# Performance work log

Hardware: AMD Instinct MI355X
Metric: run time of the kernel (lower is better)

Reference implementation:

```python
import jax, jax.numpy as jnp
import numpy as np

TOP_K = 8
N_EXPERTS = 256
N_GROUP = 8
TOPK_GROUP = 4
ROUTED_SCALING = 2.5
NORM_TOPK_PROB = True
HIDDEN = 4096
TOKENS = 16384


def setup_inputs() -> dict:
    key = jax.random.key(0)
    k1, k2, k3 = jax.random.split(key, 3)
    hidden_states = jax.random.normal(k1, (TOKENS, HIDDEN), dtype=jnp.float32)
    weight = jax.random.normal(k2, (N_EXPERTS, HIDDEN), dtype=jnp.float32) * 0.02
    e_score_correction_bias = jax.random.normal(k3, (N_EXPERTS,), dtype=jnp.float32) * 0.1
    return {
        "hidden_states": hidden_states,
        "weight": weight,
        "e_score_correction_bias": e_score_correction_bias,
    }


def _get_topk_indices(scores, bias):
    # scores: [T, E]
    T = scores.shape[0]
    scores_for_choice = scores + bias[None, :]                      # [T, E]
    grp = scores_for_choice.reshape(T, N_GROUP, N_EXPERTS // N_GROUP)
    top2_vals, _ = jax.lax.top_k(grp, 2)                            # [T, G, 2]
    group_scores = top2_vals.sum(axis=-1)                           # [T, G]
    _, group_idx = jax.lax.top_k(group_scores, TOPK_GROUP)          # [T, topk_group]
    group_mask = jnp.zeros((T, N_GROUP), dtype=scores.dtype)
    group_mask = jnp.take_along_axis(group_mask, group_idx, axis=1)  # placeholder, replaced below
    # scatter 1s into selected groups
    group_mask = jnp.zeros((T, N_GROUP), dtype=bool)
    group_mask = group_mask.at[jnp.arange(T)[:, None], group_idx].set(True)
    score_mask = jnp.repeat(group_mask, N_EXPERTS // N_GROUP, axis=1)  # [T, E]
    masked = jnp.where(score_mask, scores_for_choice, 0.0)
    _, topk_indices = jax.lax.top_k(masked, TOP_K)                  # [T, top_k]
    return topk_indices


def reference(hidden_states, weight, e_score_correction_bias):
    # router logits: [T, E]
    router_logits = jnp.einsum("th,eh->te", hidden_states.astype(jnp.float32),
                               weight.astype(jnp.float32))
    scores = jax.nn.sigmoid(router_logits)
    topk_indices = _get_topk_indices(scores, e_score_correction_bias)
    topk_weights = jnp.take_along_axis(scores, topk_indices, axis=1)  # [T, top_k]
    if NORM_TOPK_PROB:
        denom = topk_weights.sum(axis=-1, keepdims=True) + 1e-20
        topk_weights = topk_weights / denom
    topk_weights = topk_weights * ROUTED_SCALING
    return topk_indices, topk_weights.astype(jnp.float32)
```

## Files before the change

kernel.cpp:

```cpp
#include <hip/hip_runtime.h>
#include <math.h>

#define T_TOKENS 16384
#define HID      4096
#define NEXP     256
#define NGROUP   8
#define GSIZE    32
#define TOPKG    4
#define TOPK     8
#define RSCALE   2.5f

#define TAU   2e-5f
#define TAUG  3e-5f

#define BM     64
#define BK     32
#define SPLITK 4
#define KSPAN  (HID / SPLITK)
#define NKS    (KSPAN / BK)
#define NSG    (HID / BK)

#define A_HI   0
#define A_LO   2048
#define B_HI   4096
#define B_LO   12288
#define STG_TOT 20480

#define WQ_LIMB (NSG * 8192)

typedef __attribute__((ext_vector_type(8))) short bf16x8;
typedef __attribute__((ext_vector_type(4))) float f32x4;

__device__ __forceinline__ int stoffA(int r, int q) {
    return (r >> 4) * 512 + (q >> 1) * 128 + (r & 15) * 8 + (q & 1) * 4;
}
__device__ __forceinline__ int froffL(int lane) {
    return (lane >> 4) * 128 + (lane & 15) * 8;
}

__device__ __forceinline__ void gload16(const void* g, void* l) {
    __builtin_amdgcn_global_load_lds(
        (const __attribute__((address_space(1))) void*)g,
        (__attribute__((address_space(3))) void*)l, 16, 0, 0);
}

__device__ __forceinline__ void split4(const float4 v, uint& h01, uint& h23,
                                       uint& l01, uint& l23) {
    const uint u0 = __float_as_uint(v.x) + 0x8000u;
    const uint u1 = __float_as_uint(v.y) + 0x8000u;
    const uint u2 = __float_as_uint(v.z) + 0x8000u;
    const uint u3 = __float_as_uint(v.w) + 0x8000u;
    h01 = __builtin_amdgcn_perm(u1, u0, 0x07060302u);
    h23 = __builtin_amdgcn_perm(u3, u2, 0x07060302u);
    const float f0 = v.x - __uint_as_float(u0 & 0xFFFF0000u);
    const float f1 = v.y - __uint_as_float(u1 & 0xFFFF0000u);
    const float f2 = v.z - __uint_as_float(u2 & 0xFFFF0000u);
    const float f3 = v.w - __uint_as_float(u3 & 0xFFFF0000u);
    l01 = __builtin_amdgcn_perm(__float_as_uint(f1) + 0x8000u,
                                __float_as_uint(f0) + 0x8000u, 0x07060302u);
    l23 = __builtin_amdgcn_perm(__float_as_uint(f3) + 0x8000u,
                                __float_as_uint(f2) + 0x8000u, 0x07060302u);
}

template <class SC>
__device__ __forceinline__ bool route_core(SC sc, const float* __restrict__ bias,
                                           int* id, float* wv)
{
    float gs[NGROUP];
#pragma unroll
    for (int g = 0; g < NGROUP; ++g) {
        float m1 = -1e30f, m2 = -1e30f;
        for (int i = 0; i < GSIZE; ++i) {
            const int e = g * GSIZE + i;
            const float v = sc(e) + bias[e];
            if (v > m1)      { m2 = m1; m1 = v; }
            else if (v > m2) { m2 = v; }
        }
        gs[g] = m1 + m2;
    }

    unsigned gmask = 0;
    float g4 = -1e30f;
#pragma unroll
    for (int r = 0; r < TOPKG; ++r) {
        int bi = 0; float bv = -1e30f;
#pragma unroll
        for (int g = 0; g < NGROUP; ++g) {
            const bool taken = (gmask >> g) & 1;
            if (!taken && gs[g] > bv) { bv = gs[g]; bi = g; }
        }
        gmask |= 1u << bi;
        g4 = bv;
    }
    float g5 = -1e30f;
#pragma unroll
    for (int g = 0; g < NGROUP; ++g)
        if (!((gmask >> g) & 1) && gs[g] > g5) g5 = gs[g];

    float val[TOPK + 1]; int vid[TOPK + 1];
#pragma unroll
    for (int r = 0; r <= TOPK; ++r) { val[r] = -1e30f; vid[r] = 0; }
    for (int e = 0; e < NEXP; ++e) {
        const bool allowed = (gmask >> (e >> 5)) & 1;
        const float v = allowed ? (sc(e) + bias[e]) : 0.0f;
        if (v > val[TOPK]) {
#pragma unroll
            for (int p = TOPK; p >= 1; --p) {
                if (v > val[p - 1])  { val[p] = val[p - 1]; vid[p] = vid[p - 1]; }
                else if (v > val[p]) { val[p] = v;          vid[p] = e; }
            }
            if (v > val[0]) { val[0] = v; vid[0] = e; }
        }
    }

    bool tight = (g4 - g5 < TAUG);
#pragma unroll
    for (int i = 0; i < TOPK; ++i) tight |= (val[i] - val[i + 1] < TAU);

    float sum = 0.0f;
#pragma unroll
    for (int r = 0; r < TOPK; ++r) { id[r] = vid[r]; wv[r] = sc(vid[r]); sum += wv[r]; }
    const float inv = RSCALE / (sum + 1e-20f);
#pragma unroll
    for (int r = 0; r < TOPK; ++r) wv[r] *= inv;
    return tight;
}

__device__ void exact_token(const float* __restrict__ hs, const float* __restrict__ wt,
                            const float* __restrict__ bias, float* __restrict__ out, int t)
{
    float lg[NEXP];
    const float* hrow = hs + (size_t)t * HID;
    for (int e = 0; e < NEXP; ++e) {
        const float* wr = wt + (size_t)e * HID;
        float a = 0.0f;
        for (int k = 0; k < HID; k += 4) {
            const float4 x = *(const float4*)(hrow + k);
            const float4 b = *(const float4*)(wr + k);
            a = fmaf(x.x, b.x, a); a = fmaf(x.y, b.y, a);
            a = fmaf(x.z, b.z, a); a = fmaf(x.w, b.w, a);
        }
        lg[e] = 1.0f / (1.0f + expf(-a));
    }
    int id[TOPK]; float wv[TOPK];
    route_core([&](int e) { return lg[e]; }, bias, id, wv);
    for (int r = 0; r < TOPK; ++r) {
        out[(size_t)t * TOPK + r] = (float)id[r];
        out[(size_t)T_TOKENS * TOPK + (size_t)t * TOPK + r] = wv[r];
    }
}

__global__ __launch_bounds__(256, 8)
void conv_weight(const float* __restrict__ wt, ushort* __restrict__ wq)
{
    const int g  = blockIdx.x * 256 + threadIdx.x;
    const int e  = g >> 9;
    const int kc = g & 511;
    const int sg  = kc >> 2;
    const int kch = kc & 3;

    const float4 v0 = *(const float4*)(wt + (size_t)e * HID + kc * 8);
    const float4 v1 = *(const float4*)(wt + (size_t)e * HID + kc * 8 + 4);
    uint h01, h23, l01, l23, h45, h67, l45, l67;
    split4(v0, h01, h23, l01, l23);
    split4(v1, h45, h67, l45, l67);

    const size_t idx = (size_t)sg * 8192 + (size_t)((e >> 4) * 512 + kch * 128 + (e & 15) * 8);
    uint4 hv; hv.x = h01; hv.y = h23; hv.z = h45; hv.w = h67;
    uint4 lv; lv.x = l01; lv.y = l23; lv.z = l45; lv.w = l67;
    *(uint4*)&wq[idx] = hv;
    *(uint4*)&wq[(size_t)WQ_LIMB + idx] = lv;
}

__global__ __launch_bounds__(256, 4)
void router_gemm(const float* __restrict__ hs, const ushort* __restrict__ wq,
                 float* __restrict__ pw)
{
    __shared__ ushort u16[STG_TOT];

    const int tid  = threadIdx.x;
    const int lane = tid & 63;
    const int w    = tid >> 6;
    const int m    = blockIdx.x >> 2;
    const int sk   = blockIdx.x & 3;
    const int t0   = m * BM;
    const int kb0  = sk * KSPAN;
    const int r0   = tid >> 3;
    const int q    = tid & 7;

    const ushort* wq_hi = wq;
    const ushort* wq_lo = wq + WQ_LIMB;

    f32x4 acc[4][4];
#pragma unroll
    for (int i = 0; i < 4; ++i)
#pragma unroll
        for (int j = 0; j < 4; ++j) acc[i][j] = (f32x4)0.0f;

    float4 ra[2];
#pragma unroll
    for (int s = 0; s < 2; ++s)
        ra[s] = *(const float4*)(hs + (size_t)(t0 + r0 + 32 * s) * HID + kb0 + q * 4);

    for (int ks = 0; ks < NKS; ++ks) {
        const int sg = sk * NKS + ks;
        __syncthreads();

        {
            const size_t gb = (size_t)sg * 8192 + (size_t)(w * 4) * 512 + (size_t)lane * 8;
#pragma unroll
            for (int i = 0; i < 4; ++i) {
                gload16(wq_hi + gb + i * 512, &u16[B_HI + (w * 4 + i) * 512]);
                gload16(wq_lo + gb + i * 512, &u16[B_LO + (w * 4 + i) * 512]);
            }
        }
#pragma unroll
        for (int s = 0; s < 2; ++s) {
            const int r = r0 + 32 * s;
            uint h01, h23, l01, l23;
            split4(ra[s], h01, h23, l01, l23);
            const int eo = stoffA(r, q);
            uint2 hv; hv.x = h01; hv.y = h23;
            uint2 lv; lv.x = l01; lv.y = l23;
            *(uint2*)&u16[A_HI + eo] = hv;
            *(uint2*)&u16[A_LO + eo] = lv;
        }
        __syncthreads();

        if (ks + 1 < NKS) {
            const int kb = kb0 + (ks + 1) * BK;
#pragma unroll
            for (int s = 0; s < 2; ++s)
                ra[s] = *(const float4*)(hs + (size_t)(t0 + r0 + 32 * s) * HID + kb + q * 4);
        }

        const int fo = froffL(lane);
        bf16x8 ah[4], al[4];
#pragma unroll
        for (int rt = 0; rt < 4; ++rt) {
            ah[rt] = *(const bf16x8*)&u16[A_HI + rt * 512 + fo];
            al[rt] = *(const bf16x8*)&u16[A_LO + rt * 512 + fo];
        }
#pragma unroll
        for (int c = 0; c < 4; ++c) {
            const int ct = w * 4 + c;
            const bf16x8 bh = *(const bf16x8*)&u16[B_HI + ct * 512 + fo];
            const bf16x8 bl = *(const bf16x8*)&u16[B_LO + ct * 512 + fo];
#pragma unroll
            for (int rt = 0; rt < 4; ++rt) {
                acc[rt][c] = __builtin_amdgcn_mfma_f32_16x16x32_bf16(ah[rt], bh, acc[rt][c], 0, 0, 0);
                acc[rt][c] = __builtin_amdgcn_mfma_f32_16x16x32_bf16(ah[rt], bl, acc[rt][c], 0, 0, 0);
                acc[rt][c] = __builtin_amdgcn_mfma_f32_16x16x32_bf16(al[rt], bh, acc[rt][c], 0, 0, 0);
            }
        }
    }

#pragma unroll
    for (int rt = 0; rt < 4; ++rt)
#pragma unroll
        for (int c = 0; c < 4; ++c) {
            const int col  = w * 64 + c * 16 + (lane & 15);
            const int rowb = rt * 16 + (lane >> 4) * 4;
#pragma unroll
            for (int j = 0; j < 4; ++j)
                pw[((size_t)(sk * T_TOKENS) + t0 + rowb + j) * NEXP + col] = acc[rt][c][j];
        }
}

__global__ __launch_bounds__(256, 2)
void router_route(const float* __restrict__ pw, const float* __restrict__ bias,
                  float* __restrict__ out,
                  unsigned* __restrict__ wcnt, unsigned* __restrict__ wlist,
                  unsigned cap)
{
    __shared__ float Lg[NEXP * 64];
    const int tid = threadIdx.x;
    const int t0  = blockIdx.x * 64;

#pragma unroll 8
    for (int t = 0; t < 64; ++t) {
        float v = 0.0f;
#pragma unroll
        for (int s = 0; s < SPLITK; ++s)
            v += pw[((size_t)(s * T_TOKENS) + t0 + t) * NEXP + tid];
        Lg[tid * 64 + ((t + tid) & 63)] = 1.0f / (1.0f + expf(-v));
    }
    __syncthreads();

    if (tid < 64) {
        const int t = t0 + tid;
        int id[TOPK]; float wv[TOPK];
        const bool tight = route_core(
            [&](int e) { return Lg[e * 64 + ((tid + e) & 63)]; }, bias, id, wv);

#pragma unroll
        for (int r = 0; r < TOPK; ++r) {
            out[(size_t)t * TOPK + r] = (float)id[r];
            out[(size_t)T_TOKENS * TOPK + (size_t)t * TOPK + r] = wv[r];
        }
        if (tight) {
            const unsigned pos = atomicAdd(wcnt, 1u);
            if (pos < cap) wlist[pos] = (unsigned)t;
        }
    }
}

__global__ __launch_bounds__(256, 4)
void router_exact(const float* __restrict__ hs, const float* __restrict__ wt,
                  const float* __restrict__ bias, float* __restrict__ out,
                  const unsigned* __restrict__ wcnt, const unsigned* __restrict__ wlist,
                  unsigned cap)
{
    __shared__ float hrow[HID];
    __shared__ float lg[NEXP];
    const unsigned count = min(*wcnt, cap);
    const int tid  = threadIdx.x;
    const int lane = tid & 63;
    const int w    = tid >> 6;

    for (unsigned b = blockIdx.x; b < count; b += gridDim.x) {
        __syncthreads();
        const int t = (int)wlist[b];

#pragma unroll
        for (int i = 0; i < 4; ++i) {
            const int f4 = i * 256 + tid;
            *(float4*)&hrow[f4 * 4] = *(const float4*)(hs + (size_t)t * HID + f4 * 4);
        }
        __syncthreads();

        for (int g = 0; g < 16; ++g) {
            const int e0 = w * 64 + g * 4;
            float a[4] = {0.0f, 0.0f, 0.0f, 0.0f};
#pragma unroll 4
            for (int j = 0; j < 16; ++j) {
                const int f4 = j * 64 + lane;
                const float4 h = *(const float4*)&hrow[f4 * 4];
#pragma unroll
                for (int p = 0; p < 4; ++p) {
                    const float4 v = *(const float4*)(wt + (size_t)(e0 + p) * HID + f4 * 4);
                    a[p] = fmaf(h.x, v.x, a[p]); a[p] = fmaf(h.y, v.y, a[p]);
                    a[p] = fmaf(h.z, v.z, a[p]); a[p] = fmaf(h.w, v.w, a[p]);
                }
            }
#pragma unroll
            for (int p = 0; p < 4; ++p)
#pragma unroll
                for (int d = 1; d < 64; d <<= 1)
                    a[p] += __shfl_xor(a[p], d, 64);
            if (lane == 0) {
#pragma unroll
                for (int p = 0; p < 4; ++p)
                    lg[e0 + p] = 1.0f / (1.0f + expf(-a[p]));
            }
        }
        __syncthreads();

        if (tid == 0) {
            int id[TOPK]; float wv[TOPK];
            route_core([&](int e) { return lg[e]; }, bias, id, wv);
            for (int r = 0; r < TOPK; ++r) {
                out[(size_t)t * TOPK + r] = (float)id[r];
                out[(size_t)T_TOKENS * TOPK + (size_t)t * TOPK + r] = wv[r];
            }
        }
    }
}

__global__ __launch_bounds__(512, 1)
void router_mono(const float* __restrict__ hs, const float* __restrict__ wt,
                 const float* __restrict__ bias, float* __restrict__ out,
                 unsigned* __restrict__ wcnt, unsigned* __restrict__ wlist, unsigned cap)
{
    __shared__ float smem[16384];
    ushort* u16 = (ushort*)smem;
    float*  Lg  = smem;

    const int tid  = threadIdx.x;
    const int lane = tid & 63;
    const int w    = tid >> 6;
    const int t0   = blockIdx.x * 64;
    const int ar   = tid >> 3;
    const int aq   = tid & 7;

    f32x4 acc[4][2];
#pragma unroll
    for (int i = 0; i < 4; ++i)
#pragma unroll
        for (int j = 0; j < 2; ++j) acc[i][j] = (f32x4)0.0f;

    float4 ra, rb[4];
    ra = *(const float4*)(hs + (size_t)(t0 + ar) * HID + aq * 4);
#pragma unroll
    for (int s = 0; s < 4; ++s)
        rb[s] = *(const float4*)(wt + (size_t)(ar + s * 64) * HID + aq * 4);

    for (int ks = 0; ks < HID / BK; ++ks) {
        __syncthreads();
        {
            uint h01, h23, l01, l23;
            split4(ra, h01, h23, l01, l23);
            const int eo = stoffA(ar, aq);
            uint2 hv; hv.x = h01; hv.y = h23;
            uint2 lv; lv.x = l01; lv.y = l23;
            *(uint2*)&u16[0 + eo] = hv;
            *(uint2*)&u16[2048 + eo] = lv;
        }
#pragma unroll
        for (int s = 0; s < 4; ++s) {
            const int e = ar + s * 64;
            uint h01, h23, l01, l23;
            split4(rb[s], h01, h23, l01, l23);
            const int eo = stoffA(e, aq);
            uint2 hv; hv.x = h01; hv.y = h23;
            uint2 lv; lv.x = l01; lv.y = l23;
            *(uint2*)&u16[4096 + eo] = hv;
            *(uint2*)&u16[12288 + eo] = lv;
        }
        __syncthreads();
        if (ks + 1 < HID / BK) {
            const int k0 = (ks + 1) * BK;
            ra = *(const float4*)(hs + (size_t)(t0 + ar) * HID + k0 + aq * 4);
#pragma unroll
            for (int s = 0; s < 4; ++s)
                rb[s] = *(const float4*)(wt + (size_t)(ar + s * 64) * HID + k0 + aq * 4);
        }
        const int fo = froffL(lane);
        bf16x8 ah[4], al[4];
#pragma unroll
        for (int rt = 0; rt < 4; ++rt) {
            ah[rt] = *(const bf16x8*)&u16[0 + rt * 512 + fo];
            al[rt] = *(const bf16x8*)&u16[2048 + rt * 512 + fo];
        }
#pragma unroll
        for (int c = 0; c < 2; ++c) {
            const int ct = w * 2 + c;
            const bf16x8 bh = *(const bf16x8*)&u16[4096 + ct * 512 + fo];
            const bf16x8 bl = *(const bf16x8*)&u16[12288 + ct * 512 + fo];
#pragma unroll
            for (int rt = 0; rt < 4; ++rt) {
                acc[rt][c] = __builtin_amdgcn_mfma_f32_16x16x32_bf16(ah[rt], bh, acc[rt][c], 0, 0, 0);
                acc[rt][c] = __builtin_amdgcn_mfma_f32_16x16x32_bf16(ah[rt], bl, acc[rt][c], 0, 0, 0);
                acc[rt][c] = __builtin_amdgcn_mfma_f32_16x16x32_bf16(al[rt], bh, acc[rt][c], 0, 0, 0);
            }
        }
    }
    __syncthreads();
#pragma unroll
    for (int rt = 0; rt < 4; ++rt)
#pragma unroll
        for (int c = 0; c < 2; ++c) {
            const int col  = w * 32 + c * 16 + (lane & 15);
            const int rowb = rt * 16 + (lane >> 4) * 4;
#pragma unroll
            for (int j = 0; j < 4; ++j) {
                const int row = rowb + j;
                Lg[col * 64 + ((row + col) & 63)] = 1.0f / (1.0f + expf(-acc[rt][c][j]));
            }
        }
    __syncthreads();

    if (tid < 64) {
        const int t = t0 + tid;
        int id[TOPK]; float wv[TOPK];
        const bool tight = route_core(
            [&](int e) { return Lg[e * 64 + ((tid + e) & 63)]; }, bias, id, wv);
#pragma unroll
        for (int r = 0; r < TOPK; ++r) {
            out[(size_t)t * TOPK + r] = (float)id[r];
            out[(size_t)T_TOKENS * TOPK + (size_t)t * TOPK + r] = wv[r];
        }
        if (tight) {
            bool queued = false;
            if (wcnt) {
                const unsigned pos = atomicAdd(wcnt, 1u);
                if (pos < cap) { wlist[pos] = (unsigned)t; queued = true; }
            }
            if (!queued) exact_token(hs, wt, bias, out, t);
        }
    }
}

extern "C" void kernel_launch(void* const* d_in, const int* in_sizes, int n_in,
                              void* d_out, int out_size, void* d_ws, size_t ws_size,
                              hipStream_t stream) {
    const float* hs   = (const float*)d_in[0];
    const float* wt   = (const float*)d_in[1];
    const float* bias = (const float*)d_in[2];
    float* out = (float*)d_out;
    (void)in_sizes; (void)n_in; (void)out_size;

    const size_t PW_BYTES = (size_t)SPLITK * T_TOKENS * NEXP * 4;
    const size_t WQ_BYTES = (size_t)2 * WQ_LIMB * 2;
    const size_t NEED = PW_BYTES + WQ_BYTES + 4 + (size_t)T_TOKENS * 4;

    if (ws_size >= NEED) {
        float*    pw    = (float*)d_ws;
        ushort*   wq    = (ushort*)((char*)d_ws + PW_BYTES);
        unsigned* wcnt  = (unsigned*)((char*)d_ws + PW_BYTES + WQ_BYTES);
        unsigned* wlist = wcnt + 1;
        hipMemsetAsync(wcnt, 0, sizeof(unsigned), stream);
        conv_weight<<<512, 256, 0, stream>>>(wt, wq);
        router_gemm<<<(T_TOKENS / BM) * SPLITK, 256, 0, stream>>>(hs, wq, pw);
        router_route<<<T_TOKENS / 64, 256, 0, stream>>>(pw, bias, out, wcnt, wlist,
                                                        (unsigned)T_TOKENS);
        router_exact<<<2048, 256, 0, stream>>>(hs, wt, bias, out, wcnt, wlist,
                                               (unsigned)T_TOKENS);
    } else if (ws_size >= 8) {
        unsigned cap = (unsigned)((ws_size - 4) / 4);
        if (cap > T_TOKENS) cap = T_TOKENS;
        unsigned* wcnt  = (unsigned*)d_ws;
        unsigned* wlist = wcnt + 1;
        hipMemsetAsync(d_ws, 0, sizeof(unsigned), stream);
        router_mono<<<T_TOKENS / 64, 512, 0, stream>>>(hs, wt, bias, out, wcnt, wlist, cap);
        router_exact<<<2048, 256, 0, stream>>>(hs, wt, bias, out, wcnt, wlist, cap);
    } else {
        router_mono<<<T_TOKENS / 64, 512, 0, stream>>>(hs, wt, bias, out,
                                                       nullptr, nullptr, 0u);
    }
}
```

Before: 357.2 us.

## Fuse routing into split-K GEMM with last-block reduction and double-buffered LDS

Fuses the routing kernel into the GEMM: the last split-K block for each tile, found through an atomic counter, sums the partials, applies the sigmoid and runs top-k. This removes a separate kernel launch and some partial-sum traffic. Split-K drops from 4 to 2 and LDS staging becomes double-buffered, so the next tile's loads overlap with the MFMA work, which is also wrapped in s_setprio. The cost is twice the LDS, lower occupancy (launch bounds go from 4 to 2), fewer blocks, and a serialized tail in which the last block of each tile does the routing.

```diff
diff --git a/kernel.cpp b/kernel.cpp
--- a/kernel.cpp
+++ b/kernel.cpp
@@ -15,16 +15,17 @@
 
 #define BM     64
 #define BK     32
-#define SPLITK 4
+#define SPLITK 2
 #define KSPAN  (HID / SPLITK)
 #define NKS    (KSPAN / BK)
 #define NSG    (HID / BK)
+#define NMT    (T_TOKENS / BM)
 
 #define A_HI   0
 #define A_LO   2048
 #define B_HI   4096
 #define B_LO   12288
-#define STG_TOT 20480
+#define BUFSZ  20480
 
 #define WQ_LIMB (NSG * 8192)
 
@@ -172,17 +173,20 @@
     *(uint4*)&wq[(size_t)WQ_LIMB + idx] = lv;
 }
 
-__global__ __launch_bounds__(256, 4)
+__global__ __launch_bounds__(256, 2)
 void router_gemm(const float* __restrict__ hs, const ushort* __restrict__ wq,
-                 float* __restrict__ pw)
+                 const float* __restrict__ bias,
+                 float* __restrict__ pw, float* __restrict__ out,
+                 unsigned* __restrict__ cntm,
+                 unsigned* __restrict__ wcnt, unsigned* __restrict__ wlist, unsigned cap)
 {
-    __shared__ ushort u16[STG_TOT];
+    __shared__ ushort u16[2 * BUFSZ];
 
     const int tid  = threadIdx.x;
     const int lane = tid & 63;
     const int w    = tid >> 6;
-    const int m    = blockIdx.x >> 2;
-    const int sk   = blockIdx.x & 3;
+    const int m    = blockIdx.x >> 1;
+    const int sk   = blockIdx.x & 1;
     const int t0   = m * BM;
     const int kb0  = sk * KSPAN;
     const int r0   = tid >> 3;
@@ -198,54 +202,75 @@
         for (int j = 0; j < 4; ++j) acc[i][j] = (f32x4)0.0f;
 
     float4 ra[2];
-#pragma unroll
-    for (int s = 0; s < 2; ++s)
-        ra[s] = *(const float4*)(hs + (size_t)(t0 + r0 + 32 * s) * HID + kb0 + q * 4);
-
-    for (int ks = 0; ks < NKS; ++ks) {
-        const int sg = sk * NKS + ks;
-        __syncthreads();
-
-        {
-            const size_t gb = (size_t)sg * 8192 + (size_t)(w * 4) * 512 + (size_t)lane * 8;
-#pragma unroll
-            for (int i = 0; i < 4; ++i) {
-                gload16(wq_hi + gb + i * 512, &u16[B_HI + (w * 4 + i) * 512]);
-                gload16(wq_lo + gb + i * 512, &u16[B_LO + (w * 4 + i) * 512]);
-            }
+    {
+        const int sg0 = sk * NKS;
+        const size_t gb = (size_t)sg0 * 8192 + (size_t)(w * 4) * 512 + (size_t)lane * 8;
+#pragma unroll
+        for (int i = 0; i < 4; ++i) {
+            gload16(wq_hi + gb + i * 512, &u16[B_HI + (w * 4 + i) * 512]);
+            gload16(wq_lo + gb + i * 512, &u16[B_LO + (w * 4 + i) * 512]);
         }
 #pragma unroll
         for (int s = 0; s < 2; ++s) {
-            const int r = r0 + 32 * s;
+            const float4 v = *(const float4*)(hs + (size_t)(t0 + r0 + 32 * s) * HID + kb0 + q * 4);
             uint h01, h23, l01, l23;
-            split4(ra[s], h01, h23, l01, l23);
-            const int eo = stoffA(r, q);
+            split4(v, h01, h23, l01, l23);
+            const int eo = stoffA(r0 + 32 * s, q);
             uint2 hv; hv.x = h01; hv.y = h23;
             uint2 lv; lv.x = l01; lv.y = l23;
             *(uint2*)&u16[A_HI + eo] = hv;
             *(uint2*)&u16[A_LO + eo] = lv;
         }
-        __syncthreads();
+#pragma unroll
+        for (int s = 0; s < 2; ++s)
+            ra[s] = *(const float4*)(hs + (size_t)(t0 + r0 + 32 * s) * HID + kb0 + BK + q * 4);
+    }
+    __syncthreads();
+
+    int cur = 0;
+    for (int ks = 0; ks < NKS; ++ks) {
+        ushort* bc = u16 + cur * BUFSZ;
+        ushort* bn = u16 + (cur ^ 1) * BUFSZ;
 
         if (ks + 1 < NKS) {
-            const int kb = kb0 + (ks + 1) * BK;
-#pragma unroll
-            for (int s = 0; s < 2; ++s)
-                ra[s] = *(const float4*)(hs + (size_t)(t0 + r0 + 32 * s) * HID + kb + q * 4);
+            const int sg = sk * NKS + ks + 1;
+            const size_t gb = (size_t)sg * 8192 + (size_t)(w * 4) * 512 + (size_t)lane * 8;
+#pragma unroll
+            for (int i = 0; i < 4; ++i) {
+                gload16(wq_hi + gb + i * 512, bn + B_HI + (w * 4 + i) * 512);
+                gload16(wq_lo + gb + i * 512, bn + B_LO + (w * 4 + i) * 512);
+            }
+#pragma unroll
+            for (int s = 0; s < 2; ++s) {
+                uint h01, h23, l01, l23;
+                split4(ra[s], h01, h23, l01, l23);
+                const int eo = stoffA(r0 + 32 * s, q);
+                uint2 hv; hv.x = h01; hv.y = h23;
+                uint2 lv; lv.x = l01; lv.y = l23;
+                *(uint2*)&bn[A_HI + eo] = hv;
+                *(uint2*)&bn[A_LO + eo] = lv;
+            }
+            if (ks + 2 < NKS) {
+                const int kb = kb0 + (ks + 2) * BK;
+#pragma unroll
+                for (int s = 0; s < 2; ++s)
+                    ra[s] = *(const float4*)(hs + (size_t)(t0 + r0 + 32 * s) * HID + kb + q * 4);
+            }
         }
 
         const int fo = froffL(lane);
         bf16x8 ah[4], al[4];
 #pragma unroll
         for (int rt = 0; rt < 4; ++rt) {
-            ah[rt] = *(const bf16x8*)&u16[A_HI + rt * 512 + fo];
-            al[rt] = *(const bf16x8*)&u16[A_LO + rt * 512 + fo];
-        }
+            ah[rt] = *(const bf16x8*)&bc[A_HI + rt * 512 + fo];
+            al[rt] = *(const bf16x8*)&bc[A_LO + rt * 512 + fo];
+        }
+        __builtin_amdgcn_s_setprio(1);
 #pragma unroll
         for (int c = 0; c < 4; ++c) {
             const int ct = w * 4 + c;
-            const bf16x8 bh = *(const bf16x8*)&u16[B_HI + ct * 512 + fo];
-            const bf16x8 bl = *(const bf16x8*)&u16[B_LO + ct * 512 + fo];
+            const bf16x8 bh = *(const bf16x8*)&bc[B_HI + ct * 512 + fo];
+            const bf16x8 bl = *(const bf16x8*)&bc[B_LO + ct * 512 + fo];
 #pragma unroll
             for (int rt = 0; rt < 4; ++rt) {
                 acc[rt][c] = __builtin_amdgcn_mfma_f32_16x16x32_bf16(ah[rt], bh, acc[rt][c], 0, 0, 0);
@@ -253,6 +278,10 @@
                 acc[rt][c] = __builtin_amdgcn_mfma_f32_16x16x32_bf16(al[rt], bh, acc[rt][c], 0, 0, 0);
             }
         }
+        __builtin_amdgcn_s_setprio(0);
+
+        __syncthreads();
+        cur ^= 1;
     }
 
 #pragma unroll
@@ -265,42 +294,40 @@
             for (int j = 0; j < 4; ++j)
                 pw[((size_t)(sk * T_TOKENS) + t0 + rowb + j) * NEXP + col] = acc[rt][c][j];
         }
-}
-
-__global__ __launch_bounds__(256, 2)
-void router_route(const float* __restrict__ pw, const float* __restrict__ bias,
-                  float* __restrict__ out,
-                  unsigned* __restrict__ wcnt, unsigned* __restrict__ wlist,
-                  unsigned cap)
-{
-    __shared__ float Lg[NEXP * 64];
-    const int tid = threadIdx.x;
-    const int t0  = blockIdx.x * 64;
-
+
+    __threadfence();
+    __syncthreads();
+    volatile int* flag = (volatile int*)(u16 + 2 * BUFSZ - 2);
+    if (tid == 0) {
+        const unsigned old = atomicAdd(&cntm[m], 1u);
+        *flag = (old == SPLITK - 1) ? 1 : 0;
+    }
+    __syncthreads();
+    if (*flag) {
+        __threadfence();
+        float* Lg = (float*)u16;
 #pragma unroll 8
-    for (int t = 0; t < 64; ++t) {
-        float v = 0.0f;
-#pragma unroll
-        for (int s = 0; s < SPLITK; ++s)
-            v += pw[((size_t)(s * T_TOKENS) + t0 + t) * NEXP + tid];
-        Lg[tid * 64 + ((t + tid) & 63)] = 1.0f / (1.0f + expf(-v));
-    }
-    __syncthreads();
-
-    if (tid < 64) {
-        const int t = t0 + tid;
-        int id[TOPK]; float wv[TOPK];
-        const bool tight = route_core(
-            [&](int e) { return Lg[e * 64 + ((tid + e) & 63)]; }, bias, id, wv);
-
-#pragma unroll
-        for (int r = 0; r < TOPK; ++r) {
-            out[(size_t)t * TOPK + r] = (float)id[r];
-            out[(size_t)T_TOKENS * TOPK + (size_t)t * TOPK + r] = wv[r];
-        }
-        if (tight) {
-            const unsigned pos = atomicAdd(wcnt, 1u);
-            if (pos < cap) wlist[pos] = (unsigned)t;
+        for (int t = 0; t < BM; ++t) {
+            const float v = pw[((size_t)(0 * T_TOKENS) + t0 + t) * NEXP + tid]
+                          + pw[((size_t)(1 * T_TOKENS) + t0 + t) * NEXP + tid];
+            Lg[tid * 64 + ((t + tid) & 63)] = 1.0f / (1.0f + expf(-v));
+        }
+        __syncthreads();
+
+        if (tid < BM) {
+            const int t = t0 + tid;
+            int id[TOPK]; float wv[TOPK];
+            const bool tight = route_core(
+                [&](int e) { return Lg[e * 64 + ((tid + e) & 63)]; }, bias, id, wv);
+#pragma unroll
+            for (int r = 0; r < TOPK; ++r) {
+                out[(size_t)t * TOPK + r] = (float)id[r];
+                out[(size_t)T_TOKENS * TOPK + (size_t)t * TOPK + r] = wv[r];
+            }
+            if (tight) {
+                const unsigned pos = atomicAdd(wcnt, 1u);
+                if (pos < cap) wlist[pos] = (unsigned)t;
+            }
         }
     }
 }
@@ -490,20 +517,22 @@
     float* out = (float*)d_out;
     (void)in_sizes; (void)n_in; (void)out_size;
 
-    const size_t PW_BYTES = (size_t)SPLITK * T_TOKENS * NEXP * 4;
-    const size_t WQ_BYTES = (size_t)2 * WQ_LIMB * 2;
-    const size_t NEED = PW_BYTES + WQ_BYTES + 4 + (size_t)T_TOKENS * 4;
+    const size_t PW_BYTES  = (size_t)SPLITK * T_TOKENS * NEXP * 4;
+    const size_t WQ_BYTES  = (size_t)2 * WQ_LIMB * 2;
+    const size_t CTL_BYTES = 4 + (size_t)NMT * 4;
+    const size_t NEED = PW_BYTES + WQ_BYTES + CTL_BYTES + (size_t)T_TOKENS * 4;
 
     if (ws_size >= NEED) {
         float*    pw    = (float*)d_ws;
         ushort*   wq    = (ushort*)((char*)d_ws + PW_BYTES);
         unsigned* wcnt  = (unsigned*)((char*)d_ws + PW_BYTES + WQ_BYTES);
-        unsigned* wlist = wcnt + 1;
-        hipMemsetAsync(wcnt, 0, sizeof(unsigned), stream);
+        unsigned* cntm  = wcnt + 1;
+        unsigned* wlist = cntm + NMT;
+        hipMemsetAsync(wcnt, 0, CTL_BYTES, stream);
         conv_weight<<<512, 256, 0, stream>>>(wt, wq);
-        router_gemm<<<(T_TOKENS / BM) * SPLITK, 256, 0, stream>>>(hs, wq, pw);
-        router_route<<<T_TOKENS / 64, 256, 0, stream>>>(pw, bias, out, wcnt, wlist,
-                                                        (unsigned)T_TOKENS);
+        router_gemm<<<NMT * SPLITK, 256, 0, stream>>>(hs, wq, bias, pw, out,
+                                                      cntm, wcnt, wlist,
+                                                      (unsigned)T_TOKENS);
         router_exact<<<2048, 256, 0, stream>>>(hs, wt, bias, out, wcnt, wlist,
                                                (unsigned)T_TOKENS);
     } else if (ws_size >= 8) {
```

Result: slower. 472.6 us (+32.3%).

## Load GEMM operands directly into registers and batch exact-recheck tokens

Applied to the files above, without the earlier changes.

The router GEMM drops LDS staging and its two barriers per K step. Each wave now loads its pre-split bf16 weight fragments from global memory and builds the hidden-state hi/lo fragments in registers, so each wave re-reads hidden rows that other waves also read. The exact fallback kernel processes four flagged tokens per block so each weight load is reused across four rows, at the cost of more shared memory and lower occupancy. Launch bounds are lowered to match the higher register use.

```diff
diff --git a/kernel.cpp b/kernel.cpp
--- a/kernel.cpp
+++ b/kernel.cpp
@@ -20,29 +20,10 @@
 #define NKS    (KSPAN / BK)
 #define NSG    (HID / BK)
 
-#define A_HI   0
-#define A_LO   2048
-#define B_HI   4096
-#define B_LO   12288
-#define STG_TOT 20480
-
 #define WQ_LIMB (NSG * 8192)
 
 typedef __attribute__((ext_vector_type(8))) short bf16x8;
 typedef __attribute__((ext_vector_type(4))) float f32x4;
-
-__device__ __forceinline__ int stoffA(int r, int q) {
-    return (r >> 4) * 512 + (q >> 1) * 128 + (r & 15) * 8 + (q & 1) * 4;
-}
-__device__ __forceinline__ int froffL(int lane) {
-    return (lane >> 4) * 128 + (lane & 15) * 8;
-}
-
-__device__ __forceinline__ void gload16(const void* g, void* l) {
-    __builtin_amdgcn_global_load_lds(
-        (const __attribute__((address_space(1))) void*)g,
-        (__attribute__((address_space(3))) void*)l, 16, 0, 0);
-}
 
 __device__ __forceinline__ void split4(const float4 v, uint& h01, uint& h23,
                                        uint& l01, uint& l23) {
@@ -172,12 +153,10 @@
     *(uint4*)&wq[(size_t)WQ_LIMB + idx] = lv;
 }
 
-__global__ __launch_bounds__(256, 4)
+__global__ __launch_bounds__(256, 3)
 void router_gemm(const float* __restrict__ hs, const ushort* __restrict__ wq,
                  float* __restrict__ pw)
 {
-    __shared__ ushort u16[STG_TOT];
-
     const int tid  = threadIdx.x;
     const int lane = tid & 63;
     const int w    = tid >> 6;
@@ -185,8 +164,9 @@
     const int sk   = blockIdx.x & 3;
     const int t0   = m * BM;
     const int kb0  = sk * KSPAN;
-    const int r0   = tid >> 3;
-    const int q    = tid & 7;
+
+    const int row = lane & 15;
+    const int kq  = lane >> 4;
 
     const ushort* wq_hi = wq;
     const ushort* wq_lo = wq + WQ_LIMB;
@@ -197,62 +177,41 @@
 #pragma unroll
         for (int j = 0; j < 4; ++j) acc[i][j] = (f32x4)0.0f;
 
-    float4 ra[2];
-#pragma unroll
-    for (int s = 0; s < 2; ++s)
-        ra[s] = *(const float4*)(hs + (size_t)(t0 + r0 + 32 * s) * HID + kb0 + q * 4);
-
     for (int ks = 0; ks < NKS; ++ks) {
         const int sg = sk * NKS + ks;
-        __syncthreads();
-
-        {
-            const size_t gb = (size_t)sg * 8192 + (size_t)(w * 4) * 512 + (size_t)lane * 8;
-#pragma unroll
-            for (int i = 0; i < 4; ++i) {
-                gload16(wq_hi + gb + i * 512, &u16[B_HI + (w * 4 + i) * 512]);
-                gload16(wq_lo + gb + i * 512, &u16[B_LO + (w * 4 + i) * 512]);
-            }
-        }
-#pragma unroll
-        for (int s = 0; s < 2; ++s) {
-            const int r = r0 + 32 * s;
-            uint h01, h23, l01, l23;
-            split4(ra[s], h01, h23, l01, l23);
-            const int eo = stoffA(r, q);
-            uint2 hv; hv.x = h01; hv.y = h23;
-            uint2 lv; lv.x = l01; lv.y = l23;
-            *(uint2*)&u16[A_HI + eo] = hv;
-            *(uint2*)&u16[A_LO + eo] = lv;
-        }
-        __syncthreads();
-
-        if (ks + 1 < NKS) {
-            const int kb = kb0 + (ks + 1) * BK;
-#pragma unroll
-            for (int s = 0; s < 2; ++s)
-                ra[s] = *(const float4*)(hs + (size_t)(t0 + r0 + 32 * s) * HID + kb + q * 4);
-        }
-
-        const int fo = froffL(lane);
+        const int kb = kb0 + ks * BK;
+
+        bf16x8 bh[4], bl[4];
+        const size_t bb = (size_t)sg * 8192 + (size_t)(w * 4) * 512 + (size_t)lane * 8;
+#pragma unroll
+        for (int c = 0; c < 4; ++c) {
+            bh[c] = *(const bf16x8*)(wq_hi + bb + c * 512);
+            bl[c] = *(const bf16x8*)(wq_lo + bb + c * 512);
+        }
+
         bf16x8 ah[4], al[4];
 #pragma unroll
         for (int rt = 0; rt < 4; ++rt) {
-            ah[rt] = *(const bf16x8*)&u16[A_HI + rt * 512 + fo];
-            al[rt] = *(const bf16x8*)&u16[A_LO + rt * 512 + fo];
-        }
-#pragma unroll
-        for (int c = 0; c < 4; ++c) {
-            const int ct = w * 4 + c;
-            const bf16x8 bh = *(const bf16x8*)&u16[B_HI + ct * 512 + fo];
-            const bf16x8 bl = *(const bf16x8*)&u16[B_LO + ct * 512 + fo];
+            const float* ap = hs + (size_t)(t0 + rt * 16 + row) * HID + kb + kq * 8;
+            const float4 v0 = *(const float4*)ap;
+            const float4 v1 = *(const float4*)(ap + 4);
+            uint h01, h23, l01, l23, h45, h67, l45, l67;
+            split4(v0, h01, h23, l01, l23);
+            split4(v1, h45, h67, l45, l67);
+            uint4 hv; hv.x = h01; hv.y = h23; hv.z = h45; hv.w = h67;
+            uint4 lv; lv.x = l01; lv.y = l23; lv.z = l45; lv.w = l67;
+            ah[rt] = *(const bf16x8*)&hv;
+            al[rt] = *(const bf16x8*)&lv;
+        }
+
+#pragma unroll
+        for (int c = 0; c < 4; ++c)
 #pragma unroll
             for (int rt = 0; rt < 4; ++rt) {
-                acc[rt][c] = __builtin_amdgcn_mfma_f32_16x16x32_bf16(ah[rt], bh, acc[rt][c], 0, 0, 0);
-                acc[rt][c] = __builtin_amdgcn_mfma_f32_16x16x32_bf16(ah[rt], bl, acc[rt][c], 0, 0, 0);
-                acc[rt][c] = __builtin_amdgcn_mfma_f32_16x16x32_bf16(al[rt], bh, acc[rt][c], 0, 0, 0);
-            }
-        }
+                acc[rt][c] = __builtin_amdgcn_mfma_f32_16x16x32_bf16(ah[rt], bh[c], acc[rt][c], 0, 0, 0);
+                acc[rt][c] = __builtin_amdgcn_mfma_f32_16x16x32_bf16(ah[rt], bl[c], acc[rt][c], 0, 0, 0);
+                acc[rt][c] = __builtin_amdgcn_mfma_f32_16x16x32_bf16(al[rt], bh[c], acc[rt][c], 0, 0, 0);
+            }
     }
 
 #pragma unroll
@@ -305,60 +264,86 @@
     }
 }
 
-__global__ __launch_bounds__(256, 4)
+__global__ __launch_bounds__(256, 2)
 void router_exact(const float* __restrict__ hs, const float* __restrict__ wt,
                   const float* __restrict__ bias, float* __restrict__ out,
                   const unsigned* __restrict__ wcnt, const unsigned* __restrict__ wlist,
                   unsigned cap)
 {
-    __shared__ float hrow[HID];
-    __shared__ float lg[NEXP];
+    __shared__ float hrow[4][HID];
+    __shared__ float lg[4][NEXP + 1];
     const unsigned count = min(*wcnt, cap);
     const int tid  = threadIdx.x;
     const int lane = tid & 63;
     const int w    = tid >> 6;
 
-    for (unsigned b = blockIdx.x; b < count; b += gridDim.x) {
+    for (unsigned base = blockIdx.x * 4u; base < count; base += gridDim.x * 4u) {
         __syncthreads();
-        const int t = (int)wlist[b];
-
-#pragma unroll
-        for (int i = 0; i < 4; ++i) {
-            const int f4 = i * 256 + tid;
-            *(float4*)&hrow[f4 * 4] = *(const float4*)(hs + (size_t)t * HID + f4 * 4);
+        const unsigned n = (count - base < 4u) ? (count - base) : 4u;
+        int toks[4];
+#pragma unroll
+        for (int s = 0; s < 4; ++s)
+            toks[s] = (int)wlist[base + (((unsigned)s < n - 1) ? (unsigned)s : (n - 1))];
+
+#pragma unroll
+        for (int s = 0; s < 4; ++s) {
+            const float* hr = hs + (size_t)toks[s] * HID;
+#pragma unroll
+            for (int i = 0; i < 4; ++i) {
+                const int f4 = i * 256 + tid;
+                *(float4*)&hrow[s][f4 * 4] = *(const float4*)(hr + f4 * 4);
+            }
         }
         __syncthreads();
 
         for (int g = 0; g < 16; ++g) {
             const int e0 = w * 64 + g * 4;
-            float a[4] = {0.0f, 0.0f, 0.0f, 0.0f};
+            float a[4][4];
+#pragma unroll
+            for (int p = 0; p < 4; ++p)
+#pragma unroll
+                for (int t = 0; t < 4; ++t) a[p][t] = 0.0f;
+
 #pragma unroll 4
             for (int j = 0; j < 16; ++j) {
                 const int f4 = j * 64 + lane;
-                const float4 h = *(const float4*)&hrow[f4 * 4];
+                float4 h[4];
+#pragma unroll
+                for (int t = 0; t < 4; ++t)
+                    h[t] = *(const float4*)&hrow[t][f4 * 4];
 #pragma unroll
                 for (int p = 0; p < 4; ++p) {
                     const float4 v = *(const float4*)(wt + (size_t)(e0 + p) * HID + f4 * 4);
-                    a[p] = fmaf(h.x, v.x, a[p]); a[p] = fmaf(h.y, v.y, a[p]);
-                    a[p] = fmaf(h.z, v.z, a[p]); a[p] = fmaf(h.w, v.w, a[p]);
+#pragma unroll
+                    for (int t = 0; t < 4; ++t) {
+                        a[p][t] = fmaf(h[t].x, v.x, a[p][t]);
+                        a[p][t] = fmaf(h[t].y, v.y, a[p][t]);
+                        a[p][t] = fmaf(h[t].z, v.z, a[p][t]);
+                        a[p][t] = fmaf(h[t].w, v.w, a[p][t]);
+                    }
                 }
             }
 #pragma unroll
             for (int p = 0; p < 4; ++p)
 #pragma unroll
-                for (int d = 1; d < 64; d <<= 1)
-                    a[p] += __shfl_xor(a[p], d, 64);
+                for (int t = 0; t < 4; ++t)
+#pragma unroll
+                    for (int d = 1; d < 64; d <<= 1)
+                        a[p][t] += __shfl_xor(a[p][t], d, 64);
             if (lane == 0) {
 #pragma unroll
-                for (int p = 0; p < 4; ++p)
-                    lg[e0 + p] = 1.0f / (1.0f + expf(-a[p]));
+                for (int t = 0; t < 4; ++t)
+#pragma unroll
+                    for (int p = 0; p < 4; ++p)
+                        lg[t][e0 + p] = 1.0f / (1.0f + expf(-a[p][t]));
             }
         }
         __syncthreads();
 
-        if (tid == 0) {
+        if (tid < (int)n) {
+            const int t = toks[tid];
             int id[TOPK]; float wv[TOPK];
-            route_core([&](int e) { return lg[e]; }, bias, id, wv);
+            route_core([&](int e) { return lg[tid][e]; }, bias, id, wv);
             for (int r = 0; r < TOPK; ++r) {
                 out[(size_t)t * TOPK + r] = (float)id[r];
                 out[(size_t)T_TOKENS * TOPK + (size_t)t * TOPK + r] = wv[r];
@@ -400,7 +385,7 @@
         {
             uint h01, h23, l01, l23;
             split4(ra, h01, h23, l01, l23);
-            const int eo = stoffA(ar, aq);
+            const int eo = (ar >> 4) * 512 + (aq >> 1) * 128 + (ar & 15) * 8 + (aq & 1) * 4;
             uint2 hv; hv.x = h01; hv.y = h23;
             uint2 lv; lv.x = l01; lv.y = l23;
             *(uint2*)&u16[0 + eo] = hv;
@@ -411,7 +396,7 @@
             const int e = ar + s * 64;
             uint h01, h23, l01, l23;
             split4(rb[s], h01, h23, l01, l23);
-            const int eo = stoffA(e, aq);
+            const int eo = (e >> 4) * 512 + (aq >> 1) * 128 + (e & 15) * 8 + (aq & 1) * 4;
             uint2 hv; hv.x = h01; hv.y = h23;
             uint2 lv; lv.x = l01; lv.y = l23;
             *(uint2*)&u16[4096 + eo] = hv;
@@ -425,7 +410,7 @@
             for (int s = 0; s < 4; ++s)
                 rb[s] = *(const float4*)(wt + (size_t)(ar + s * 64) * HID + k0 + aq * 4);
         }
-        const int fo = froffL(lane);
+        const int fo = (lane >> 4) * 128 + (lane & 15) * 8;
         bf16x8 ah[4], al[4];
 #pragma unroll
         for (int rt = 0; rt < 4; ++rt) {
```

Result: slower. 536.2 us (+50.1%).

## Fuse split-K reduction and routing into GEMM via last-arriver atomic counter

Applied to the files above, without the earlier changes.

Removes the separate router_route launch. The last split-K block for each token tile, found through a per-tile atomic counter, now sums the partials, applies sigmoid and runs grouped top-k inside the GEMM kernel, reusing its shared staging buffer in two 32-token halves. This cuts one kernel launch and lets routing overlap with other tiles' GEMM work, at the cost of threadfences, extra atomics and a serialized tail in the last-arriving block. The ambiguity thresholds TAU and TAUG are also tightened, so fewer tokens should fall back to the exact recompute path, with some risk to correctness margin.

```diff
diff --git a/kernel.cpp b/kernel.cpp
--- a/kernel.cpp
+++ b/kernel.cpp
@@ -10,8 +10,8 @@
 #define TOPK     8
 #define RSCALE   2.5f
 
-#define TAU   2e-5f
-#define TAUG  3e-5f
+#define TAU   1.5e-5f
+#define TAUG  2.5e-5f
 
 #define BM     64
 #define BK     32
@@ -19,12 +19,14 @@
 #define KSPAN  (HID / SPLITK)
 #define NKS    (KSPAN / BK)
 #define NSG    (HID / BK)
+#define NMT    (T_TOKENS / BM)
 
 #define A_HI   0
 #define A_LO   2048
 #define B_HI   4096
 #define B_LO   12288
 #define STG_TOT 20480
+#define FLAG_U16 20476
 
 #define WQ_LIMB (NSG * 8192)
 
@@ -174,7 +176,10 @@
 
 __global__ __launch_bounds__(256, 4)
 void router_gemm(const float* __restrict__ hs, const ushort* __restrict__ wq,
-                 float* __restrict__ pw)
+                 const float* __restrict__ bias,
+                 float* __restrict__ pw, float* __restrict__ out,
+                 unsigned* __restrict__ cntm,
+                 unsigned* __restrict__ wcnt, unsigned* __restrict__ wlist, unsigned cap)
 {
     __shared__ ushort u16[STG_TOT];
 
@@ -265,42 +270,47 @@
             for (int j = 0; j < 4; ++j)
                 pw[((size_t)(sk * T_TOKENS) + t0 + rowb + j) * NEXP + col] = acc[rt][c][j];
         }
-}
-
-__global__ __launch_bounds__(256, 2)
-void router_route(const float* __restrict__ pw, const float* __restrict__ bias,
-                  float* __restrict__ out,
-                  unsigned* __restrict__ wcnt, unsigned* __restrict__ wlist,
-                  unsigned cap)
-{
-    __shared__ float Lg[NEXP * 64];
-    const int tid = threadIdx.x;
-    const int t0  = blockIdx.x * 64;
-
+
+    __threadfence();
+    __syncthreads();
+    volatile int* flag = (volatile int*)&u16[FLAG_U16];
+    if (tid == 0) {
+        const unsigned old = atomicAdd(&cntm[m], 1u);
+        *flag = (old == SPLITK - 1) ? 1 : 0;
+    }
+    __syncthreads();
+    if (*flag) {
+        __threadfence();
+        float* Lg = (float*)u16;
+#pragma unroll
+        for (int h = 0; h < 2; ++h) {
+            __syncthreads();
 #pragma unroll 8
-    for (int t = 0; t < 64; ++t) {
-        float v = 0.0f;
-#pragma unroll
-        for (int s = 0; s < SPLITK; ++s)
-            v += pw[((size_t)(s * T_TOKENS) + t0 + t) * NEXP + tid];
-        Lg[tid * 64 + ((t + tid) & 63)] = 1.0f / (1.0f + expf(-v));
-    }
-    __syncthreads();
-
-    if (tid < 64) {
-        const int t = t0 + tid;
-        int id[TOPK]; float wv[TOPK];
-        const bool tight = route_core(
-            [&](int e) { return Lg[e * 64 + ((tid + e) & 63)]; }, bias, id, wv);
-
-#pragma unroll
-        for (int r = 0; r < TOPK; ++r) {
-            out[(size_t)t * TOPK + r] = (float)id[r];
-            out[(size_t)T_TOKENS * TOPK + (size_t)t * TOPK + r] = wv[r];
-        }
-        if (tight) {
-            const unsigned pos = atomicAdd(wcnt, 1u);
-            if (pos < cap) wlist[pos] = (unsigned)t;
+            for (int t = 0; t < 32; ++t) {
+                const int row = t0 + h * 32 + t;
+                float v = 0.0f;
+#pragma unroll
+                for (int s = 0; s < SPLITK; ++s)
+                    v += pw[((size_t)(s * T_TOKENS) + row) * NEXP + tid];
+                Lg[tid * 32 + ((t + tid) & 31)] = 1.0f / (1.0f + expf(-v));
+            }
+            __syncthreads();
+
+            if (tid < 32) {
+                const int t = t0 + h * 32 + tid;
+                int id[TOPK]; float wv[TOPK];
+                const bool tight = route_core(
+                    [&](int e) { return Lg[e * 32 + ((tid + e) & 31)]; }, bias, id, wv);
+#pragma unroll
+                for (int r = 0; r < TOPK; ++r) {
+                    out[(size_t)t * TOPK + r] = (float)id[r];
+                    out[(size_t)T_TOKENS * TOPK + (size_t)t * TOPK + r] = wv[r];
+                }
+                if (tight) {
+                    const unsigned pos = atomicAdd(wcnt, 1u);
+                    if (pos < cap) wlist[pos] = (unsigned)t;
+                }
+            }
         }
     }
 }
@@ -490,20 +500,22 @@
     float* out = (float*)d_out;
     (void)in_sizes; (void)n_in; (void)out_size;
 
-    const size_t PW_BYTES = (size_t)SPLITK * T_TOKENS * NEXP * 4;
-    const size_t WQ_BYTES = (size_t)2 * WQ_LIMB * 2;
-    const size_t NEED = PW_BYTES + WQ_BYTES + 4 + (size_t)T_TOKENS * 4;
+    const size_t PW_BYTES  = (size_t)SPLITK * T_TOKENS * NEXP * 4;
+    const size_t WQ_BYTES  = (size_t)2 * WQ_LIMB * 2;
+    const size_t CTL_BYTES = 4 + (size_t)NMT * 4;
+    const size_t NEED = PW_BYTES + WQ_BYTES + CTL_BYTES + (size_t)T_TOKENS * 4;
 
     if (ws_size >= NEED) {
         float*    pw    = (float*)d_ws;
         ushort*   wq    = (ushort*)((char*)d_ws + PW_BYTES);
         unsigned* wcnt  = (unsigned*)((char*)d_ws + PW_BYTES + WQ_BYTES);
-        unsigned* wlist = wcnt + 1;
-        hipMemsetAsync(wcnt, 0, sizeof(unsigned), stream);
+        unsigned* cntm  = wcnt + 1;
+        unsigned* wlist = cntm + NMT;
+        hipMemsetAsync(wcnt, 0, CTL_BYTES, stream);
         conv_weight<<<512, 256, 0, stream>>>(wt, wq);
-        router_gemm<<<(T_TOKENS / BM) * SPLITK, 256, 0, stream>>>(hs, wq, pw);
-        router_route<<<T_TOKENS / 64, 256, 0, stream>>>(pw, bias, out, wcnt, wlist,
-                                                        (unsigned)T_TOKENS);
+        router_gemm<<<NMT * SPLITK, 256, 0, stream>>>(hs, wq, bias, pw, out,
+                                                      cntm, wcnt, wlist,
+                                                      (unsigned)T_TOKENS);
         router_exact<<<2048, 256, 0, stream>>>(hs, wt, bias, out, wcnt, wlist,
                                                (unsigned)T_TOKENS);
     } else if (ws_size >= 8) {
```

Measured after the change: 665.4 us. +86.3%, slower.
